# Kernel tuning notes

Measured on AMD Instinct MI355X. Metric: run time of the kernel, lower is better.

## Reference

```python
import jax, jax.numpy as jnp
import numpy as np

N = 50000
E = 500000
IN_DIM = 384
HID = 128
HEADS = 4
OUT_DIM = 384
NEG_SLOPE = 0.2


def gat_conv(x, edge_index, W, att_src, att_dst, bias):
    """PyG GATConv (concat=True, add_self_loops=True, eval mode).
    x: [N, F_in]; edge_index: [2, E] (row 0 = source j, row 1 = target i);
    W: [F_in, H*C]; att_src/att_dst: [H, C]; bias: [H*C].
    """
    n = x.shape[0]
    # add self loops
    loops = jnp.arange(n, dtype=edge_index.dtype)
    src = jnp.concatenate([edge_index[0], loops])
    dst = jnp.concatenate([edge_index[1], loops])

    h = (x @ W).reshape(n, HEADS, -1)              # [N, H, C]
    a_src = jnp.einsum('nhc,hc->nh', h, att_src)   # [N, H]
    a_dst = jnp.einsum('nhc,hc->nh', h, att_dst)   # [N, H]

    e = a_src[src] + a_dst[dst]                    # [E', H]
    e = jax.nn.leaky_relu(e, NEG_SLOPE)
    # segment softmax over incoming edges of each target node
    e_max = jax.ops.segment_max(e, dst, num_segments=n)
    e_exp = jnp.exp(e - e_max[dst])
    denom = jax.ops.segment_sum(e_exp, dst, num_segments=n)
    alpha = e_exp / denom[dst]                     # [E', H]

    msg = h[src] * alpha[:, :, None]               # [E', H, C]
    out = jax.ops.segment_sum(msg, dst, num_segments=n)  # [N, H, C]
    return out.reshape(n, -1) + bias


def setup_inputs() -> dict:
    key = jax.random.key(0)
    ks = jax.random.split(key, 12)
    s_in = 1.0 / np.sqrt(IN_DIM)
    s_h = 1.0 / np.sqrt(HEADS * HID)
    return {
        'x': jax.random.normal(ks[0], (N, IN_DIM), dtype=jnp.float32),
        'edge_index': jax.random.randint(ks[1], (2, E), 0, N, dtype=jnp.int32),
        'W1': jax.random.normal(ks[2], (IN_DIM, HEADS * HID), dtype=jnp.float32) * s_in,
        'a1_src': jax.random.normal(ks[3], (HEADS, HID), dtype=jnp.float32) * s_in,
        'a1_dst': jax.random.normal(ks[4], (HEADS, HID), dtype=jnp.float32) * s_in,
        'b1': jnp.zeros((HEADS * HID,), dtype=jnp.float32),
        'W2': jax.random.normal(ks[5], (HEADS * HID, HEADS * HID), dtype=jnp.float32) * s_h,
        'a2_src': jax.random.normal(ks[6], (HEADS, HID), dtype=jnp.float32) * s_h,
        'a2_dst': jax.random.normal(ks[7], (HEADS, HID), dtype=jnp.float32) * s_h,
        'b2': jnp.zeros((HEADS * HID,), dtype=jnp.float32),
        'Wfc': jax.random.normal(ks[8], (HEADS * HID, OUT_DIM), dtype=jnp.float32) * s_h,
        'bfc': jnp.zeros((OUT_DIM,), dtype=jnp.float32),
    }


def reference(x, edge_index, W1, a1_src, a1_dst, b1, W2, a2_src, a2_dst, b2, Wfc, bfc):
    h = jax.nn.relu(gat_conv(x, edge_index, W1, a1_src, a1_dst, b1))
    h = jax.nn.relu(gat_conv(h, edge_index, W2, a2_src, a2_dst, b2))
    return h @ Wfc + bfc  # [N, OUT_DIM]
```

## Files before the change

### kernel.cpp

```cpp
#include <hip/hip_runtime.h>
#include <cfloat>
#include <cstdint>

#define HEADS 4
#define HIDC 128
#define HC 512
#define NEG 0.2f

typedef _Float16 half8 __attribute__((ext_vector_type(8)));
typedef float floatx4 __attribute__((ext_vector_type(4)));

__global__ __launch_bounds__(256) void mfma_gemm(
    const _Float16* __restrict__ A,
    const _Float16* __restrict__ Bt,
    _Float16* __restrict__ Ch,
    float* __restrict__ Cf,
    const float* __restrict__ bias,
    const float* __restrict__ atts,
    const float* __restrict__ attd,
    float* __restrict__ a_src,
    float* __restrict__ a_dst,
    int M, int N, int K)
{
    __shared__ __align__(16) _Float16 As[128 * 32];
    __shared__ __align__(16) _Float16 Bs[128 * 32];

    const int nwg = gridDim.x * gridDim.y;
    int lin = blockIdx.y * gridDim.x + blockIdx.x;
    {
        const int q = nwg >> 3, r = nwg & 7;
        const int xcd = lin & 7, pos = lin >> 3;
        lin = (xcd < r ? xcd * (q + 1) : r * (q + 1) + (xcd - r) * q) + pos;
    }
    const int bx = lin % gridDim.x;
    const int by = lin / gridDim.x;

    const int tid = threadIdx.x;
    const int w = tid >> 6;
    const int lane = tid & 63;
    const int wr = (w >> 1) * 64;
    const int wc = (w & 1) * 64;

    const int rowBase = by * 128;
    const int colBase = bx * 128;

    const int sRow0 = (w * 2 + 0) * 16 + (lane >> 2);
    const int sRow1 = (w * 2 + 1) * 16 + (lane >> 2);
    const int sCol = (lane & 3) * 8;

    const _Float16* gA0 = A + (size_t)(rowBase + sRow0) * K + sCol;
    const _Float16* gA1 = A + (size_t)(rowBase + sRow1) * K + sCol;
    const _Float16* gB0 = Bt + (size_t)(colBase + sRow0) * K + sCol;
    const _Float16* gB1 = Bt + (size_t)(colBase + sRow1) * K + sCol;

    _Float16* lA0 = &As[(w * 2 + 0) * 512];
    _Float16* lA1 = &As[(w * 2 + 1) * 512];
    _Float16* lB0 = &Bs[(w * 2 + 0) * 512];
    _Float16* lB1 = &Bs[(w * 2 + 1) * 512];

    floatx4 acc[4][4];
#pragma unroll
    for (int i = 0; i < 4; i++)
#pragma unroll
        for (int j = 0; j < 4; j++) acc[i][j] = {0.f, 0.f, 0.f, 0.f};

    const int q16 = lane >> 4;
    const int l16 = lane & 15;

    for (int k0 = 0; k0 < K; k0 += 32) {
        __builtin_amdgcn_global_load_lds(
            (const __attribute__((address_space(1))) unsigned int*)(gA0 + k0),
            (__attribute__((address_space(3))) unsigned int*)lA0, 16, 0, 0);
        __builtin_amdgcn_global_load_lds(
            (const __attribute__((address_space(1))) unsigned int*)(gA1 + k0),
            (__attribute__((address_space(3))) unsigned int*)lA1, 16, 0, 0);
        __builtin_amdgcn_global_load_lds(
            (const __attribute__((address_space(1))) unsigned int*)(gB0 + k0),
            (__attribute__((address_space(3))) unsigned int*)lB0, 16, 0, 0);
        __builtin_amdgcn_global_load_lds(
            (const __attribute__((address_space(1))) unsigned int*)(gB1 + k0),
            (__attribute__((address_space(3))) unsigned int*)lB1, 16, 0, 0);
        __syncthreads();

        half8 af[4], bf[4];
#pragma unroll
        for (int i = 0; i < 4; i++)
            af[i] = *(const half8*)&As[(wr + i * 16 + l16) * 32 + q16 * 8];
#pragma unroll
        for (int j = 0; j < 4; j++)
            bf[j] = *(const half8*)&Bs[(wc + j * 16 + l16) * 32 + q16 * 8];
#pragma unroll
        for (int i = 0; i < 4; i++)
#pragma unroll
            for (int j = 0; j < 4; j++)
                acc[i][j] = __builtin_amdgcn_mfma_f32_16x16x32_f16(af[i], bf[j], acc[i][j], 0, 0, 0);
        __syncthreads();
    }

    if (Ch) {
#pragma unroll
        for (int i = 0; i < 4; i++)
#pragma unroll
            for (int j = 0; j < 4; j++) {
                const int col = colBase + wc + j * 16 + l16;
#pragma unroll
                for (int r = 0; r < 4; r++) {
                    const int row = rowBase + wr + i * 16 + q16 * 4 + r;
                    if (row < M) Ch[(size_t)row * N + col] = (_Float16)acc[i][j][r];
                }
            }
    }
    if (Cf) {
#pragma unroll
        for (int i = 0; i < 4; i++)
#pragma unroll
            for (int j = 0; j < 4; j++) {
                const int col = colBase + wc + j * 16 + l16;
                const float bb = bias ? bias[col] : 0.f;
#pragma unroll
                for (int r = 0; r < 4; r++) {
                    const int row = rowBase + wr + i * 16 + q16 * 4 + r;
                    if (row < M) Cf[(size_t)row * N + col] = acc[i][j][r] + bb;
                }
            }
    }

    if (atts) {
        float* ps = (float*)As;
        float* pd = ps + 256;
        const int head = bx;
        float as[4], ad[4];
#pragma unroll
        for (int j = 0; j < 4; j++) {
            const int cl = wc + j * 16 + l16;
            as[j] = atts[head * HIDC + cl];
            ad[j] = attd[head * HIDC + cl];
        }
#pragma unroll
        for (int i = 0; i < 4; i++) {
#pragma unroll
            for (int r = 0; r < 4; r++) {
                float s_ = acc[i][0][r] * as[0] + acc[i][1][r] * as[1]
                         + acc[i][2][r] * as[2] + acc[i][3][r] * as[3];
                float d_ = acc[i][0][r] * ad[0] + acc[i][1][r] * ad[1]
                         + acc[i][2][r] * ad[2] + acc[i][3][r] * ad[3];
#pragma unroll
                for (int mk = 1; mk <= 8; mk <<= 1) {
                    s_ += __shfl_xor(s_, mk);
                    d_ += __shfl_xor(d_, mk);
                }
                if (l16 == 0) {
                    const int rloc = wr + i * 16 + q16 * 4 + r;
                    ps[(wc >> 6) * 128 + rloc] = s_;
                    pd[(wc >> 6) * 128 + rloc] = d_;
                }
            }
        }
        __syncthreads();
        if (tid < 128) {
            const int row = rowBase + tid;
            if (row < M) {
                a_src[(size_t)row * 4 + head] = ps[tid] + ps[128 + tid];
                a_dst[(size_t)row * 4 + head] = pd[tid] + pd[128 + tid];
            }
        }
    }
}

__global__ void convert_x_kernel(const float* __restrict__ x, _Float16* __restrict__ o, size_t nquads)
{
    size_t i = (size_t)blockIdx.x * blockDim.x + threadIdx.x;
    if (i < nquads) {
        float4 v = *(const float4*)(x + i * 4);
        _Float16* p = o + i * 4;
        p[0] = (_Float16)v.x; p[1] = (_Float16)v.y;
        p[2] = (_Float16)v.z; p[3] = (_Float16)v.w;
    }
}

__global__ void convert_wT_kernel(const float* __restrict__ W, _Float16* __restrict__ Wt, int K, int N)
{
    int k = blockIdx.x * 64 + (threadIdx.x & 63);
    int n = blockIdx.y * 4 + (threadIdx.x >> 6);
    if (k < K && n < N) Wt[(size_t)n * K + k] = (_Float16)W[(size_t)k * N + n];
}

__global__ void count_kernel(const int* __restrict__ dst, int* __restrict__ deg, int E)
{
    int e = blockIdx.x * blockDim.x + threadIdx.x;
    if (e < E) atomicAdd(&deg[dst[e]], 1);
}

__global__ __launch_bounds__(256) void block_sum_kernel(
    const int* __restrict__ deg, int* __restrict__ bsum, int Nn)
{
    int gid = blockIdx.x * 256 + threadIdx.x;
    int v = (gid < Nn) ? deg[gid] : 0;
#pragma unroll
    for (int o = 32; o >= 1; o >>= 1) v += __shfl_xor(v, o);
    __shared__ int ws[4];
    if ((threadIdx.x & 63) == 0) ws[threadIdx.x >> 6] = v;
    __syncthreads();
    if (threadIdx.x == 0) bsum[blockIdx.x] = ws[0] + ws[1] + ws[2] + ws[3];
}

__global__ __launch_bounds__(256) void scan_bsum_kernel(
    const int* __restrict__ bsum, int* __restrict__ bbase, int nb)
{
    __shared__ int s[256];
    const int tid = threadIdx.x;
    int v = (tid < nb) ? bsum[tid] : 0;
    s[tid] = v;
    __syncthreads();
    for (int off = 1; off < 256; off <<= 1) {
        int t = (tid >= off) ? s[tid - off] : 0;
        __syncthreads();
        s[tid] += t;
        __syncthreads();
    }
    if (tid < nb) bbase[tid] = s[tid] - v;
}

__global__ __launch_bounds__(256) void fill_rowptr_kernel(
    const int* __restrict__ deg, const int* __restrict__ bbase,
    int* __restrict__ rowptr, int* __restrict__ cursor, int Nn, int E)
{
    __shared__ int s[256];
    const int tid = threadIdx.x;
    const int gid = blockIdx.x * 256 + tid;
    int v = (gid < Nn) ? deg[gid] : 0;
    s[tid] = v;
    __syncthreads();
    for (int off = 1; off < 256; off <<= 1) {
        int t = (tid >= off) ? s[tid - off] : 0;
        __syncthreads();
        s[tid] += t;
        __syncthreads();
    }
    if (gid < Nn) {
        int r = bbase[blockIdx.x] + s[tid] - v;
        rowptr[gid] = r;
        cursor[gid] = r;
    }
    if (gid == 0) rowptr[Nn] = E;
}

__global__ void fill_kernel(const int* __restrict__ src, const int* __restrict__ dst,
                            int* __restrict__ cursor, int* __restrict__ eidx, int E)
{
    int e = blockIdx.x * blockDim.x + threadIdx.x;
    if (e < E) {
        int d = dst[e];
        int pos = atomicAdd(&cursor[d], 1);
        eidx[pos] = src[e];
    }
}

__global__ __launch_bounds__(256) void gather_kernel(
    const _Float16* __restrict__ h, const float* __restrict__ a_src,
    const float* __restrict__ a_dst,
    const int* __restrict__ rowptr, const int* __restrict__ eidx,
    const float* __restrict__ bias, _Float16* __restrict__ out, int Nn)
{
    const int wv = __builtin_amdgcn_readfirstlane(threadIdx.x >> 6);
    const int node = blockIdx.x * 4 + wv;
    if (node >= Nn) return;
    const int lane = threadIdx.x & 63;
    const int hd = lane >> 4;

    const int beg = rowptr[node];
    const int deg = rowptr[node + 1] - beg;
    const int total = deg + 1;

    const float ad = a_dst[(size_t)node * 4 + hd];
    const _Float16* hb = h + (size_t)lane * 8;

    float acc[8];
#pragma unroll
    for (int i = 0; i < 8; i++) acc[i] = 0.f;
    float dsum = 0.f;

    for (int base = 0; base < total; base += 64) {
        const int cnt = min(total - base, 64);
        const int t = base + lane;
        int myIdx = node;
        if (t < deg) myIdx = eidx[beg + t];

        for (int e = 0; e < cnt; e += 4) {
            const int s0 = __shfl(myIdx, e);
            const int s1 = __shfl(myIdx, e + 1);
            const int s2 = __shfl(myIdx, e + 2);
            const int s3 = __shfl(myIdx, e + 3);
            half8 hv0 = *(const half8*)(hb + (size_t)s0 * HC);
            half8 hv1 = *(const half8*)(hb + (size_t)s1 * HC);
            half8 hv2 = *(const half8*)(hb + (size_t)s2 * HC);
            half8 hv3 = *(const half8*)(hb + (size_t)s3 * HC);
            const float as0 = a_src[(size_t)s0 * 4 + hd];
            const float as1 = a_src[(size_t)s1 * 4 + hd];
            const float as2 = a_src[(size_t)s2 * 4 + hd];
            const float as3 = a_src[(size_t)s3 * 4 + hd];
            float l0 = as0 + ad; l0 = l0 > 0.f ? l0 : NEG * l0;
            float l1 = as1 + ad; l1 = l1 > 0.f ? l1 : NEG * l1;
            float l2 = as2 + ad; l2 = l2 > 0.f ? l2 : NEG * l2;
            float l3 = as3 + ad; l3 = l3 > 0.f ? l3 : NEG * l3;
            const float w0 = __expf(l0);
            const float w1 = (e + 1 < cnt) ? __expf(l1) : 0.f;
            const float w2 = (e + 2 < cnt) ? __expf(l2) : 0.f;
            const float w3 = (e + 3 < cnt) ? __expf(l3) : 0.f;
            dsum += (w0 + w1) + (w2 + w3);
#pragma unroll
            for (int i = 0; i < 8; i++)
                acc[i] += (w0 * (float)hv0[i] + w1 * (float)hv1[i])
                        + (w2 * (float)hv2[i] + w3 * (float)hv3[i]);
        }
    }

    const float is = 1.f / dsum;
    const float* bp = bias + lane * 8;
    half8 ov;
#pragma unroll
    for (int i = 0; i < 8; i++) {
        float o = acc[i] * is + bp[i];
        o = o > 0.f ? o : 0.f;
        ov[i] = (_Float16)o;
    }
    *(half8*)(out + (size_t)node * HC + (size_t)lane * 8) = ov;
}

extern "C" void kernel_launch(void* const* d_in, const int* in_sizes, int n_in,
                              void* d_out, int out_size, void* d_ws, size_t ws_size,
                              hipStream_t stream)
{
    const float* x   = (const float*)d_in[0];
    const int*   ei  = (const int*)d_in[1];
    const float* W1  = (const float*)d_in[2];
    const float* a1s = (const float*)d_in[3];
    const float* a1d = (const float*)d_in[4];
    const float* b1  = (const float*)d_in[5];
    const float* W2  = (const float*)d_in[6];
    const float* a2s = (const float*)d_in[7];
    const float* a2d = (const float*)d_in[8];
    const float* b2  = (const float*)d_in[9];
    const float* Wfc = (const float*)d_in[10];
    const float* bfc = (const float*)d_in[11];
    float* out = (float*)d_out;

    const int Nn  = in_sizes[0] / 384;
    const int E   = in_sizes[1] / 2;
    const int IN  = 384;
    const int OUT = in_sizes[11];
    const int Mp  = ((Nn + 127) / 128) * 128;
    const int nb  = (Nn + 255) / 256;

    uint8_t* p = (uint8_t*)d_ws;
    auto alloc = [&](size_t bytes) {
        uint8_t* r = p;
        p += (bytes + 255) & ~(size_t)255;
        return r;
    };
    _Float16* Ah_x = (_Float16*)alloc((size_t)Mp * IN * 2);
    _Float16* Ah_g = (_Float16*)alloc((size_t)Mp * HC * 2);
    _Float16* Hh   = (_Float16*)alloc((size_t)Mp * HC * 2);
    _Float16* Wt1  = (_Float16*)alloc((size_t)HC * IN * 2);
    _Float16* Wt2  = (_Float16*)alloc((size_t)HC * HC * 2);
    _Float16* Wt3  = (_Float16*)alloc((size_t)OUT * HC * 2);
    float* a_src   = (float*)alloc((size_t)Nn * 4 * 4);
    float* a_dst   = (float*)alloc((size_t)Nn * 4 * 4);
    int* deg       = (int*)alloc((size_t)Nn * 4);
    int* rowptr    = (int*)alloc((size_t)(Nn + 1) * 4);
    int* cursor    = (int*)alloc((size_t)Nn * 4);
    int* eidx      = (int*)alloc((size_t)E * 4);
    int* bsum      = (int*)alloc((size_t)nb * 4);
    int* bbase     = (int*)alloc((size_t)nb * 4);

    const int* e_src = ei;
    const int* e_dst = ei + E;

    {
        size_t nq = (size_t)Nn * IN / 4;
        convert_x_kernel<<<(nq + 255) / 256, 256, 0, stream>>>(x, Ah_x, nq);
        dim3 gw1((IN + 63) / 64, HC / 4);
        convert_wT_kernel<<<gw1, 256, 0, stream>>>(W1, Wt1, IN, HC);
        dim3 gw2((HC + 63) / 64, HC / 4);
        convert_wT_kernel<<<gw2, 256, 0, stream>>>(W2, Wt2, HC, HC);
        dim3 gw3((HC + 63) / 64, OUT / 4);
        convert_wT_kernel<<<gw3, 256, 0, stream>>>(Wfc, Wt3, HC, OUT);
    }

    hipMemsetAsync(deg, 0, Nn * sizeof(int), stream);
    const int eb = (E + 255) / 256;
    count_kernel<<<eb, 256, 0, stream>>>(e_dst, deg, E);
    block_sum_kernel<<<nb, 256, 0, stream>>>(deg, bsum, Nn);
    scan_bsum_kernel<<<1, 256, 0, stream>>>(bsum, bbase, nb);
    fill_rowptr_kernel<<<nb, 256, 0, stream>>>(deg, bbase, rowptr, cursor, Nn, E);
    fill_kernel<<<eb, 256, 0, stream>>>(e_src, e_dst, cursor, eidx, E);

    const dim3 gg1(HC / 128, Mp / 128);
    const int gb = (Nn + 3) / 4;

    mfma_gemm<<<gg1, 256, 0, stream>>>(Ah_x, Wt1, Hh, nullptr, nullptr,
                                       a1s, a1d, a_src, a_dst, Nn, HC, IN);
    gather_kernel<<<gb, 256, 0, stream>>>(Hh, a_src, a_dst, rowptr, eidx, b1, Ah_g, Nn);

    mfma_gemm<<<gg1, 256, 0, stream>>>(Ah_g, Wt2, Hh, nullptr, nullptr,
                                       a2s, a2d, a_src, a_dst, Nn, HC, HC);
    gather_kernel<<<gb, 256, 0, stream>>>(Hh, a_src, a_dst, rowptr, eidx, b2, Ah_g, Nn);

    const dim3 gg3(OUT / 128, Mp / 128);
    mfma_gemm<<<gg3, 256, 0, stream>>>(Ah_g, Wt3, nullptr, out, bfc,
                                       nullptr, nullptr, nullptr, nullptr, Nn, OUT, HC);
}
```

Baseline: 549.3 us.

## Double GEMM K-tile with XOR-swizzled LDS, merge weight converts, shrink gather blocks

The MFMA GEMM now stages a 64-wide K slice per iteration into an XOR-swizzled LDS layout. This halves the number of barrier pairs and is meant to avoid LDS bank conflicts on the half8 fragment reads. The three weight transpose/convert launches are merged into one 3D-grid kernel. The gather kernel drops from 256 to 128 threads per block (2 nodes per block) to give the scheduler finer-grained work. In exchange, LDS use per block doubles and more blocks are launched for the gather.

```diff
diff --git a/kernel.cpp b/kernel.cpp
--- a/kernel.cpp
+++ b/kernel.cpp
@@ -22,8 +22,8 @@
     float* __restrict__ a_dst,
     int M, int N, int K)
 {
-    __shared__ __align__(16) _Float16 As[128 * 32];
-    __shared__ __align__(16) _Float16 Bs[128 * 32];
+    __shared__ __align__(16) _Float16 As[128 * 64];
+    __shared__ __align__(16) _Float16 Bs[128 * 64];
 
     const int nwg = gridDim.x * gridDim.y;
     int lin = blockIdx.y * gridDim.x + blockIdx.x;
@@ -44,19 +44,8 @@
     const int rowBase = by * 128;
     const int colBase = bx * 128;
 
-    const int sRow0 = (w * 2 + 0) * 16 + (lane >> 2);
-    const int sRow1 = (w * 2 + 1) * 16 + (lane >> 2);
-    const int sCol = (lane & 3) * 8;
-
-    const _Float16* gA0 = A + (size_t)(rowBase + sRow0) * K + sCol;
-    const _Float16* gA1 = A + (size_t)(rowBase + sRow1) * K + sCol;
-    const _Float16* gB0 = Bt + (size_t)(colBase + sRow0) * K + sCol;
-    const _Float16* gB1 = Bt + (size_t)(colBase + sRow1) * K + sCol;
-
-    _Float16* lA0 = &As[(w * 2 + 0) * 512];
-    _Float16* lA1 = &As[(w * 2 + 1) * 512];
-    _Float16* lB0 = &Bs[(w * 2 + 0) * 512];
-    _Float16* lB1 = &Bs[(w * 2 + 1) * 512];
+    const int strow = lane >> 3;
+    const int sColSw = (((lane & 7) ^ strow) * 8);
 
     floatx4 acc[4][4];
 #pragma unroll
@@ -67,33 +56,40 @@
     const int q16 = lane >> 4;
     const int l16 = lane & 15;
 
-    for (int k0 = 0; k0 < K; k0 += 32) {
-        __builtin_amdgcn_global_load_lds(
-            (const __attribute__((address_space(1))) unsigned int*)(gA0 + k0),
-            (__attribute__((address_space(3))) unsigned int*)lA0, 16, 0, 0);
-        __builtin_amdgcn_global_load_lds(
-            (const __attribute__((address_space(1))) unsigned int*)(gA1 + k0),
-            (__attribute__((address_space(3))) unsigned int*)lA1, 16, 0, 0);
-        __builtin_amdgcn_global_load_lds(
-            (const __attribute__((address_space(1))) unsigned int*)(gB0 + k0),
-            (__attribute__((address_space(3))) unsigned int*)lB0, 16, 0, 0);
-        __builtin_amdgcn_global_load_lds(
-            (const __attribute__((address_space(1))) unsigned int*)(gB1 + k0),
-            (__attribute__((address_space(3))) unsigned int*)lB1, 16, 0, 0);
-        __syncthreads();
-
-        half8 af[4], bf[4];
-#pragma unroll
-        for (int i = 0; i < 4; i++)
-            af[i] = *(const half8*)&As[(wr + i * 16 + l16) * 32 + q16 * 8];
-#pragma unroll
-        for (int j = 0; j < 4; j++)
-            bf[j] = *(const half8*)&Bs[(wc + j * 16 + l16) * 32 + q16 * 8];
-#pragma unroll
-        for (int i = 0; i < 4; i++)
-#pragma unroll
-            for (int j = 0; j < 4; j++)
-                acc[i][j] = __builtin_amdgcn_mfma_f32_16x16x32_f16(af[i], bf[j], acc[i][j], 0, 0, 0);
+    for (int k0 = 0; k0 < K; k0 += 64) {
+#pragma unroll
+        for (int c = 0; c < 4; c++) {
+            const int rr = (c * 4 + w) * 8;
+            const _Float16* ga = A + (size_t)(rowBase + rr + strow) * K + k0 + sColSw;
+            const _Float16* gb = Bt + (size_t)(colBase + rr + strow) * K + k0 + sColSw;
+            __builtin_amdgcn_global_load_lds(
+                (const __attribute__((address_space(1))) unsigned int*)ga,
+                (__attribute__((address_space(3))) unsigned int*)&As[rr * 64], 16, 0, 0);
+            __builtin_amdgcn_global_load_lds(
+                (const __attribute__((address_space(1))) unsigned int*)gb,
+                (__attribute__((address_space(3))) unsigned int*)&Bs[rr * 64], 16, 0, 0);
+        }
+        __syncthreads();
+
+#pragma unroll
+        for (int s = 0; s < 2; s++) {
+            half8 af[4], bf[4];
+#pragma unroll
+            for (int i = 0; i < 4; i++) {
+                const int r = wr + i * 16 + l16;
+                af[i] = *(const half8*)&As[r * 64 + (((s * 4 + q16) ^ (r & 7)) * 8)];
+            }
+#pragma unroll
+            for (int j = 0; j < 4; j++) {
+                const int r = wc + j * 16 + l16;
+                bf[j] = *(const half8*)&Bs[r * 64 + (((s * 4 + q16) ^ (r & 7)) * 8)];
+            }
+#pragma unroll
+            for (int i = 0; i < 4; i++)
+#pragma unroll
+                for (int j = 0; j < 4; j++)
+                    acc[i][j] = __builtin_amdgcn_mfma_f32_16x16x32_f16(af[i], bf[j], acc[i][j], 0, 0, 0);
+        }
         __syncthreads();
     }
 
@@ -178,11 +174,18 @@
     }
 }
 
-__global__ void convert_wT_kernel(const float* __restrict__ W, _Float16* __restrict__ Wt, int K, int N)
-{
+__global__ void convert_wT3_kernel(
+    const float* __restrict__ W1, const float* __restrict__ W2, const float* __restrict__ W3,
+    _Float16* __restrict__ T1, _Float16* __restrict__ T2, _Float16* __restrict__ T3)
+{
+    const int z = blockIdx.z;
+    const float* W = (z == 0) ? W1 : (z == 1) ? W2 : W3;
+    _Float16* T = (z == 0) ? T1 : (z == 1) ? T2 : T3;
+    const int K = (z == 0) ? 384 : 512;
+    const int N = (z == 2) ? 384 : 512;
     int k = blockIdx.x * 64 + (threadIdx.x & 63);
     int n = blockIdx.y * 4 + (threadIdx.x >> 6);
-    if (k < K && n < N) Wt[(size_t)n * K + k] = (_Float16)W[(size_t)k * N + n];
+    if (k < K && n < N) T[(size_t)n * K + k] = (_Float16)W[(size_t)k * N + n];
 }
 
 __global__ void count_kernel(const int* __restrict__ dst, int* __restrict__ deg, int E)
@@ -256,14 +259,14 @@
     }
 }
 
-__global__ __launch_bounds__(256) void gather_kernel(
+__global__ __launch_bounds__(128) void gather_kernel(
     const _Float16* __restrict__ h, const float* __restrict__ a_src,
     const float* __restrict__ a_dst,
     const int* __restrict__ rowptr, const int* __restrict__ eidx,
     const float* __restrict__ bias, _Float16* __restrict__ out, int Nn)
 {
     const int wv = __builtin_amdgcn_readfirstlane(threadIdx.x >> 6);
-    const int node = blockIdx.x * 4 + wv;
+    const int node = blockIdx.x * 2 + wv;
     if (node >= Nn) return;
     const int lane = threadIdx.x & 63;
     const int hd = lane >> 4;
@@ -379,12 +382,8 @@
     {
         size_t nq = (size_t)Nn * IN / 4;
         convert_x_kernel<<<(nq + 255) / 256, 256, 0, stream>>>(x, Ah_x, nq);
-        dim3 gw1((IN + 63) / 64, HC / 4);
-        convert_wT_kernel<<<gw1, 256, 0, stream>>>(W1, Wt1, IN, HC);
-        dim3 gw2((HC + 63) / 64, HC / 4);
-        convert_wT_kernel<<<gw2, 256, 0, stream>>>(W2, Wt2, HC, HC);
-        dim3 gw3((HC + 63) / 64, OUT / 4);
-        convert_wT_kernel<<<gw3, 256, 0, stream>>>(Wfc, Wt3, HC, OUT);
+        dim3 gw(8, 128, 3);
+        convert_wT3_kernel<<<gw, 256, 0, stream>>>(W1, W2, Wfc, Wt1, Wt2, Wt3);
     }
 
     hipMemsetAsync(deg, 0, Nn * sizeof(int), stream);
@@ -396,15 +395,15 @@
     fill_kernel<<<eb, 256, 0, stream>>>(e_src, e_dst, cursor, eidx, E);
 
     const dim3 gg1(HC / 128, Mp / 128);
-    const int gb = (Nn + 3) / 4;
+    const int gb = (Nn + 1) / 2;
 
     mfma_gemm<<<gg1, 256, 0, stream>>>(Ah_x, Wt1, Hh, nullptr, nullptr,
                                        a1s, a1d, a_src, a_dst, Nn, HC, IN);
-    gather_kernel<<<gb, 256, 0, stream>>>(Hh, a_src, a_dst, rowptr, eidx, b1, Ah_g, Nn);
+    gather_kernel<<<gb, 128, 0, stream>>>(Hh, a_src, a_dst, rowptr, eidx, b1, Ah_g, Nn);
 
     mfma_gemm<<<gg1, 256, 0, stream>>>(Ah_g, Wt2, Hh, nullptr, nullptr,
                                        a2s, a2d, a_src, a_dst, Nn, HC, HC);
-    gather_kernel<<<gb, 256, 0, stream>>>(Hh, a_src, a_dst, rowptr, eidx, b2, Ah_g, Nn);
+    gather_kernel<<<gb, 128, 0, stream>>>(Hh, a_src, a_dst, rowptr, eidx, b2, Ah_g, Nn);
 
     const dim3 gg3(OUT / 128, Mp / 128);
     mfma_gemm<<<gg3, 256, 0, stream>>>(Ah_g, Wt3, nullptr, out, bfc,
```

After: 536.8 us. 2.3% less time.
